# Performance work log

Hardware: AMD Instinct MI355X
Metric: run time of the kernel (lower is better)

The kernel has to match this reference:

```python
import jax, jax.numpy as jnp
import numpy as np

B, M, H = 8192, 512, 1024
CORRUPTION_LEN = int(0.6 * M)  # int(corruption_rate * input_dim)


def setup_inputs() -> dict:
    key = jax.random.key(0)
    ks = jax.random.split(key, 10)
    anchor = jax.random.normal(ks[0], (B, M), jnp.float32)
    random_sample = jax.random.normal(ks[1], (B, M), jnp.float32)
    # per-row random permutation -> exactly CORRUPTION_LEN corrupted features per row
    u = jax.random.uniform(ks[2], (B, M))
    ranks = jnp.argsort(jnp.argsort(u, axis=1), axis=1)  # rank of each column in a random permutation
    corruption_mask = ranks < CORRUPTION_LEN
    s_in = 1.0 / np.sqrt(M)
    s_h = 1.0 / np.sqrt(H)
    enc_w0 = jax.random.normal(ks[3], (M, H), jnp.float32) * s_in
    enc_b0 = jnp.full((H,), 0.01, jnp.float32)
    enc_w = jax.random.normal(ks[4], (3, H, H), jnp.float32) * s_h
    enc_b = jnp.full((3, H), 0.01, jnp.float32)
    head_w = jax.random.normal(ks[5], (2, H, H), jnp.float32) * s_h
    head_b = jnp.full((2, H), 0.01, jnp.float32)
    return {
        "anchor": anchor,
        "random_sample": random_sample,
        "corruption_mask": corruption_mask,
        "enc_w0": enc_w0,
        "enc_b0": enc_b0,
        "enc_w": enc_w,
        "enc_b": enc_b,
        "head_w": head_w,
        "head_b": head_b,
    }


def _mlp(x, w0, b0, ws, bs):
    # first dense + relu
    h = jax.nn.relu(x @ w0 + b0)
    # remaining dense + relu layers (small fixed count)
    for i in range(ws.shape[0]):
        h = jax.nn.relu(h @ ws[i] + bs[i])
    return h


def _embed(x, enc_w0, enc_b0, enc_w, enc_b, head_w, head_b):
    h = _mlp(x, enc_w0, enc_b0, enc_w, enc_b)          # encoder: 4 dense+relu
    h = jax.nn.relu(h @ head_w[0] + head_b[0])          # head: 2 dense+relu
    h = jax.nn.relu(h @ head_w[1] + head_b[1])
    return h


def reference(anchor, random_sample, corruption_mask, enc_w0, enc_b0, enc_w, enc_b, head_w, head_b):
    positive = jnp.where(corruption_mask, random_sample, anchor)
    emb_anchor = _embed(anchor, enc_w0, enc_b0, enc_w, enc_b, head_w, head_b)
    emb_positive = _embed(positive, enc_w0, enc_b0, enc_w, enc_b, head_w, head_b)
    return (emb_anchor, emb_positive)
```

## Files before the change

### kernel.cpp

```cpp
#include <hip/hip_runtime.h>
#include <hip/hip_bf16.h>
#include <stdint.h>


typedef __bf16 bf16x8 __attribute__((ext_vector_type(8)));
typedef float  f32x4  __attribute__((ext_vector_type(4)));
typedef unsigned short u16x8 __attribute__((ext_vector_type(8)));

__device__ __forceinline__ void gload_lds16(const void* g, void* l) {
  __builtin_amdgcn_global_load_lds(
      (const __attribute__((address_space(1))) uint32_t*)g,
      (__attribute__((address_space(3))) uint32_t*)l, 16, 0, 0);
}

__device__ __forceinline__ void fsplit(float v, uint16_t& ho, uint16_t& lo) {
  __bf16 hb = (__bf16)v;
  float  r  = v - (float)hb;
  __bf16 lb = (__bf16)r;
  ho = __builtin_bit_cast(uint16_t, hb);
  lo = __builtin_bit_cast(uint16_t, lb);
}

__global__ void detect_mask_kernel(const uint8_t* __restrict__ mask,
                                   int* __restrict__ flag) {
  if (threadIdx.x == 0 && blockIdx.x == 0) {
    uint32_t or_hi = 0;
    for (int i = 0; i < 256; ++i)
      or_hi |= ((const uint32_t*)mask)[i] & 0xFFFFFF00u;
    *flag = (or_hi != 0) ? 1 : 0;
  }
}

__global__ void pack_kernel(const float* __restrict__ anchor,
                            const float* __restrict__ rnd,
                            const uint8_t* __restrict__ mask,
                            const int* __restrict__ mask_is_bytes,
                            uint16_t* __restrict__ Xop) {
  int t = blockIdx.x * 256 + threadIdx.x;
  int row = t >> 6;
  int idx = t & 63;
  int g = idx >> 2, c = idx & 3;
  int kbase = idx * 8;
  const float4* ap = (const float4*)(anchor + (size_t)row * 512 + kbase);
  const float4* rp = (const float4*)(rnd + (size_t)row * 512 + kbase);
  float a[8], r[8];
  *(float4*)&a[0] = ap[0]; *(float4*)&a[4] = ap[1];
  *(float4*)&r[0] = rp[0]; *(float4*)&r[4] = rp[1];
  uint32_t mb;
  if (*mask_is_bytes) {
    const uint32_t* mp = (const uint32_t*)(mask + (size_t)row * 512 + kbase);
    uint32_t w0 = mp[0], w1 = mp[1];
    mb = 0;
#pragma unroll
    for (int j = 0; j < 4; ++j) {
      mb |= ((w0 >> (8 * j)) & 1u) << j;
      mb |= ((w1 >> (8 * j)) & 1u) << (4 + j);
    }
  } else {
    const int* mi = (const int*)mask + (size_t)row * 512 + kbase;
    int4 m0 = ((const int4*)mi)[0], m1 = ((const int4*)mi)[1];
    mb = (m0.x ? 1u : 0) | (m0.y ? 2u : 0) | (m0.z ? 4u : 0) | (m0.w ? 8u : 0) |
         (m1.x ? 16u : 0) | (m1.y ? 32u : 0) | (m1.z ? 64u : 0) | (m1.w ? 128u : 0);
  }
  u16x8 ah, al, ph, pl;
#pragma unroll
  for (int j = 0; j < 8; ++j) {
    uint16_t h, lo;
    fsplit(a[j], h, lo); ah[j] = h; al[j] = lo;
    float pv = ((mb >> j) & 1u) ? r[j] : a[j];
    fsplit(pv, h, lo); ph[j] = h; pl[j] = lo;
  }
  int s = row & 7;
  size_t base = ((size_t)row * 16 + g) * 64;
  *(u16x8*)(Xop + base + (size_t)((c ^ s)) * 8) = ah;
  *(u16x8*)(Xop + base + (size_t)(((c + 4) ^ s)) * 8) = al;
  size_t pbase = ((size_t)(row + 8192) * 16 + g) * 64;
  *(u16x8*)(Xop + pbase + (size_t)((c ^ s)) * 8) = ph;
  *(u16x8*)(Xop + pbase + (size_t)(((c + 4) ^ s)) * 8) = pl;
}

__global__ void wprep_kernel(const float* __restrict__ W,
                             uint16_t* __restrict__ Bop, int K) {
  __shared__ float tbuf[32][33];
  int g = blockIdx.x, n0 = blockIdx.y * 32;
  int tid = threadIdx.x;
#pragma unroll
  for (int i = 0; i < 4; ++i)
    tbuf[(tid >> 5) + i * 8][tid & 31] =
        W[((size_t)g * 32 + (tid >> 5) + i * 8) * 1024 + n0 + (tid & 31)];
  __syncthreads();
  if (tid < 128) {
    int nl = tid >> 2, c = tid & 3;
    int n = n0 + nl, s = n & 7;
    u16x8 hi, lo;
#pragma unroll
    for (int j = 0; j < 8; ++j) {
      uint16_t h, l2;
      fsplit(tbuf[c * 8 + j][nl], h, l2);
      hi[j] = h; lo[j] = l2;
    }
    size_t base = ((size_t)n * (K / 32) + g) * 64;
    *(u16x8*)(Bop + base + (size_t)((c ^ s)) * 8) = hi;
    *(u16x8*)(Bop + base + (size_t)(((c + 4) ^ s)) * 8) = lo;
  }
}

__device__ __forceinline__ void mfma_row(f32x4* accrow, bf16x8 aH, bf16x8 aL,
                                         const bf16x8* bh, const bf16x8* bl) {
#pragma unroll
  for (int n = 0; n < 4; ++n) {
    accrow[n] = __builtin_amdgcn_mfma_f32_16x16x32_bf16(aH, bh[n], accrow[n], 0, 0, 0);
    accrow[n] = __builtin_amdgcn_mfma_f32_16x16x32_bf16(aH, bl[n], accrow[n], 0, 0, 0);
    accrow[n] = __builtin_amdgcn_mfma_f32_16x16x32_bf16(aL, bh[n], accrow[n], 0, 0, 0);
  }
}

template <int K, bool LAST>
__global__ __launch_bounds__(512, 2) void gemm_kernel(
    const uint16_t* __restrict__ Aop, const uint16_t* __restrict__ Bop,
    const float* __restrict__ bias,
    uint16_t* __restrict__ Yop, float* __restrict__ Yf) {
  constexpr int KG = K / 32;
  __shared__ uint16_t sA[2][256 * 64];
  __shared__ uint16_t sB[2][256 * 64];

  int bid = blockIdx.x;
  int xcd = bid & 7, lid = bid >> 3;
  int tm = xcd * 8 + (lid >> 2), tn = lid & 3;
  const int brow = tm * 256, bcol = tn * 256;

  const int tid = threadIdx.x;
  const int l = tid & 63, w = tid >> 6;
  const int wr = w >> 2, wc = w & 3;
  const int l15 = l & 15, c16 = l >> 4;

  f32x4 acc[8][4];
#pragma unroll
  for (int m = 0; m < 8; ++m)
#pragma unroll
    for (int n = 0; n < 4; ++n) acc[m][n] = 0;

#define STAGE_A(g_, buf_)                                                     \
  _Pragma("unroll") for (int i = 0; i < 4; ++i) {                             \
    int row_ = i * 64 + (tid >> 3);                                           \
    gload_lds16(Aop + ((size_t)(brow + row_) * KG + (g_)) * 64 + (tid & 7) * 8,\
                &sA[buf_][i * 4096 + tid * 8]);                               \
  }
#define STAGE_B(g_, buf_)                                                     \
  _Pragma("unroll") for (int i = 0; i < 4; ++i) {                             \
    int row_ = i * 64 + (tid >> 3);                                           \
    gload_lds16(Bop + ((size_t)(bcol + row_) * KG + (g_)) * 64 + (tid & 7) * 8,\
                &sB[buf_][i * 4096 + tid * 8]);                               \
  }
#define READ_A(mm, aH, aL)                                                    \
  {                                                                           \
    int fr_ = wr * 128 + (mm)*16 + l15;                                       \
    const uint16_t* rp_ = pA + fr_ * 64;                                      \
    aH = *(const bf16x8*)(rp_ + ((c16 ^ (fr_ & 7))) * 8);                     \
    aL = *(const bf16x8*)(rp_ + (((c16 + 4) ^ (fr_ & 7))) * 8);               \
  }
#define BARRIER() __builtin_amdgcn_s_barrier()
#define VM0()                                                                 \
  asm volatile("s_waitcnt vmcnt(0)" ::: "memory");                            \
  __builtin_amdgcn_sched_barrier(0)

  STAGE_A(0, 0)
  STAGE_B(0, 0)
  VM0();
  BARRIER();

  int cur = 0;
#pragma unroll 1
  for (int g = 0; g < KG; ++g) {
    const uint16_t* pA = &sA[cur][0];
    const uint16_t* pB = &sB[cur][0];
    const bool pf = (g + 1 < KG);
    const int nxt = cur ^ 1;

    if (pf) { STAGE_A(g + 1, nxt) }

    bf16x8 bh[4], bl[4];
#pragma unroll
    for (int n = 0; n < 4; ++n) {
      int fc = wc * 64 + n * 16 + l15;
      const uint16_t* rp = pB + fc * 64;
      bh[n] = *(const bf16x8*)(rp + ((c16 ^ (fc & 7))) * 8);
      bl[n] = *(const bf16x8*)(rp + (((c16 + 4) ^ (fc & 7))) * 8);
    }
    bf16x8 a0h, a0l, a1h, a1l, a2h, a2l, a3h, a3l;
    READ_A(0, a0h, a0l)
    READ_A(1, a1h, a1l)
    READ_A(2, a2h, a2l)
    READ_A(3, a3h, a3l)
    __builtin_amdgcn_s_setprio(1);
    mfma_row(acc[0], a0h, a0l, bh, bl);
    mfma_row(acc[1], a1h, a1l, bh, bl);
    __builtin_amdgcn_s_setprio(0);
    if (pf) { STAGE_B(g + 1, nxt) }
    READ_A(4, a0h, a0l)
    READ_A(5, a1h, a1l)
    __builtin_amdgcn_s_setprio(1);
    mfma_row(acc[2], a2h, a2l, bh, bl);
    mfma_row(acc[3], a3h, a3l, bh, bl);
    __builtin_amdgcn_s_setprio(0);
    READ_A(6, a2h, a2l)
    READ_A(7, a3h, a3l)
    __builtin_amdgcn_s_setprio(1);
    mfma_row(acc[4], a0h, a0l, bh, bl);
    mfma_row(acc[5], a1h, a1l, bh, bl);
    mfma_row(acc[6], a2h, a2l, bh, bl);
    mfma_row(acc[7], a3h, a3l, bh, bl);
    __builtin_amdgcn_s_setprio(0);

    VM0();
    BARRIER();
    cur = nxt;
  }

  float bb[4];
  int colg[4], colc[4], cole[4];
#pragma unroll
  for (int n = 0; n < 4; ++n) {
    int col = bcol + wc * 64 + n * 16 + l15;
    bb[n] = bias[col];
    colg[n] = col >> 5; colc[n] = (col >> 3) & 3; cole[n] = col & 7;
  }
#pragma unroll
  for (int m = 0; m < 8; ++m) {
#pragma unroll
    for (int j = 0; j < 4; ++j) {
      int rowY = brow + wr * 128 + m * 16 + c16 * 4 + j;
      int s = rowY & 7;
#pragma unroll
      for (int n = 0; n < 4; ++n) {
        float v = acc[m][n][j] + bb[n];
        v = v > 0.f ? v : 0.f;
        if (LAST) {
          Yf[(size_t)rowY * 1024 + bcol + wc * 64 + n * 16 + l15] = v;
        } else {
          uint16_t h, lo2;
          fsplit(v, h, lo2);
          size_t base = ((size_t)rowY * 32 + colg[n]) * 64;
          Yop[base + (size_t)((colc[n] ^ s)) * 8 + cole[n]] = h;
          Yop[base + (size_t)(((colc[n] + 4) ^ s)) * 8 + cole[n]] = lo2;
        }
      }
    }
  }
#undef STAGE_A
#undef STAGE_B
#undef READ_A
#undef BARRIER
#undef VM0
}

extern "C" void kernel_launch(void* const* d_in, const int* in_sizes, int n_in,
                              void* d_out, int out_size, void* d_ws, size_t ws_size,
                              hipStream_t stream) {
  (void)in_sizes; (void)n_in; (void)out_size; (void)ws_size;
  const float*   anchor = (const float*)d_in[0];
  const float*   rnd    = (const float*)d_in[1];
  const uint8_t* mask   = (const uint8_t*)d_in[2];
  const float*   enc_w0 = (const float*)d_in[3];
  const float*   enc_b0 = (const float*)d_in[4];
  const float*   enc_w  = (const float*)d_in[5];
  const float*   enc_b  = (const float*)d_in[6];
  const float*   head_w = (const float*)d_in[7];
  const float*   head_b = (const float*)d_in[8];
  float* out = (float*)d_out;

  const size_t WSZ0 = (size_t)512 * 2048;
  const size_t WSZ1 = (size_t)1024 * 2048;
  uint16_t* Wop = (uint16_t*)d_ws;
  size_t WOFF[6];
  WOFF[0] = 0;
  WOFF[1] = WSZ0;
  for (int i = 2; i < 6; ++i) WOFF[i] = WOFF[i - 1] + WSZ1;
  uint16_t* Xop = Wop + WOFF[5] + WSZ1;
  uint16_t* Yop = Xop + (size_t)16384 * 1024;
  int* mflag = (int*)(Yop + (size_t)16384 * 2048);
  uint16_t* Zop = (uint16_t*)d_out;

  detect_mask_kernel<<<1, 64, 0, stream>>>(mask, mflag);

  pack_kernel<<<2048, 256, 0, stream>>>(anchor, rnd, mask, mflag, Xop);

  wprep_kernel<<<dim3(16, 32), 256, 0, stream>>>(enc_w0, Wop + WOFF[0], 512);
  for (int i = 0; i < 3; ++i)
    wprep_kernel<<<dim3(32, 32), 256, 0, stream>>>(enc_w + (size_t)i * 1048576,
                                                   Wop + WOFF[1 + i], 1024);
  for (int i = 0; i < 2; ++i)
    wprep_kernel<<<dim3(32, 32), 256, 0, stream>>>(head_w + (size_t)i * 1048576,
                                                   Wop + WOFF[4 + i], 1024);

  dim3 g(256), b(512);
  gemm_kernel<512,  false><<<g, b, 0, stream>>>(Xop, Wop + WOFF[0], enc_b0,        Yop, nullptr);
  gemm_kernel<1024, false><<<g, b, 0, stream>>>(Yop, Wop + WOFF[1], enc_b,         Zop, nullptr);
  gemm_kernel<1024, false><<<g, b, 0, stream>>>(Zop, Wop + WOFF[2], enc_b + 1024,  Yop, nullptr);
  gemm_kernel<1024, false><<<g, b, 0, stream>>>(Yop, Wop + WOFF[3], enc_b + 2048,  Zop, nullptr);
  gemm_kernel<1024, false><<<g, b, 0, stream>>>(Zop, Wop + WOFF[4], head_b,        Yop, nullptr);
  gemm_kernel<1024, true ><<<g, b, 0, stream>>>(Yop, Wop + WOFF[5], head_b + 1024, nullptr, out);
}
```

Before: 627.1 us.

## Switch GEMM to 128x128 tiles with 32x32x16 MFMA and ping-pong barriers

Shrinks the GEMM block tile from 256x256 with 512 threads to 128x128 with 256 threads. Each wave now computes a 64x64 sub-tile with 32x32x16 bf16 MFMAs instead of 16x16x32, and the grid grows fourfold. Extra barriers and lgkmcnt waits are added between the LDS fragment reads and the MFMA clusters, so that waves in a block alternate between memory and compute phases. Smaller tiles lower the arithmetic intensity per block and raise global and L2 traffic, in exchange for more resident blocks and fewer registers per wave.

Measured after the change: 784.1 us. +25.0%, slower.

```diff
diff --git a/kernel.cpp b/kernel.cpp
--- a/kernel.cpp
+++ b/kernel.cpp
@@ -4,7 +4,7 @@
 
 
 typedef __bf16 bf16x8 __attribute__((ext_vector_type(8)));
-typedef float  f32x4  __attribute__((ext_vector_type(4)));
+typedef float  f32x16 __attribute__((ext_vector_type(16)));
 typedef unsigned short u16x8 __attribute__((ext_vector_type(8)));
 
 __device__ __forceinline__ void gload_lds16(const void* g, void* l) {
@@ -105,64 +105,62 @@
   }
 }
 
-__device__ __forceinline__ void mfma_row(f32x4* accrow, bf16x8 aH, bf16x8 aL,
-                                         const bf16x8* bh, const bf16x8* bl) {
-#pragma unroll
-  for (int n = 0; n < 4; ++n) {
-    accrow[n] = __builtin_amdgcn_mfma_f32_16x16x32_bf16(aH, bh[n], accrow[n], 0, 0, 0);
-    accrow[n] = __builtin_amdgcn_mfma_f32_16x16x32_bf16(aH, bl[n], accrow[n], 0, 0, 0);
-    accrow[n] = __builtin_amdgcn_mfma_f32_16x16x32_bf16(aL, bh[n], accrow[n], 0, 0, 0);
-  }
-}
-
 template <int K, bool LAST>
-__global__ __launch_bounds__(512, 2) void gemm_kernel(
+__global__ __launch_bounds__(256, 2) void gemm_kernel(
     const uint16_t* __restrict__ Aop, const uint16_t* __restrict__ Bop,
     const float* __restrict__ bias,
     uint16_t* __restrict__ Yop, float* __restrict__ Yf) {
   constexpr int KG = K / 32;
-  __shared__ uint16_t sA[2][256 * 64];
-  __shared__ uint16_t sB[2][256 * 64];
+  __shared__ uint16_t sA[2][128 * 64];
+  __shared__ uint16_t sB[2][128 * 64];
 
   int bid = blockIdx.x;
   int xcd = bid & 7, lid = bid >> 3;
-  int tm = xcd * 8 + (lid >> 2), tn = lid & 3;
-  const int brow = tm * 256, bcol = tn * 256;
+  int tm = xcd * 16 + (lid >> 3), tn = lid & 7;
+  const int brow = tm * 128, bcol = tn * 128;
 
   const int tid = threadIdx.x;
   const int l = tid & 63, w = tid >> 6;
-  const int wr = w >> 2, wc = w & 3;
-  const int l15 = l & 15, c16 = l >> 4;
-
-  f32x4 acc[8][4];
-#pragma unroll
-  for (int m = 0; m < 8; ++m)
-#pragma unroll
-    for (int n = 0; n < 4; ++n) acc[m][n] = 0;
+  const int wr = w >> 1, wc = w & 1;
+  const int l31 = l & 31, lh = l >> 5;
+
+  f32x16 acc[2][2];
+#pragma unroll
+  for (int m = 0; m < 2; ++m)
+#pragma unroll
+    for (int n = 0; n < 2; ++n) acc[m][n] = 0;
 
 #define STAGE_A(g_, buf_)                                                     \
   _Pragma("unroll") for (int i = 0; i < 4; ++i) {                             \
-    int row_ = i * 64 + (tid >> 3);                                           \
+    int row_ = i * 32 + (tid >> 3);                                           \
     gload_lds16(Aop + ((size_t)(brow + row_) * KG + (g_)) * 64 + (tid & 7) * 8,\
-                &sA[buf_][i * 4096 + tid * 8]);                               \
+                &sA[buf_][i * 2048 + tid * 8]);                               \
   }
 #define STAGE_B(g_, buf_)                                                     \
   _Pragma("unroll") for (int i = 0; i < 4; ++i) {                             \
-    int row_ = i * 64 + (tid >> 3);                                           \
+    int row_ = i * 32 + (tid >> 3);                                           \
     gload_lds16(Bop + ((size_t)(bcol + row_) * KG + (g_)) * 64 + (tid & 7) * 8,\
-                &sB[buf_][i * 4096 + tid * 8]);                               \
-  }
-#define READ_A(mm, aH, aL)                                                    \
+                &sB[buf_][i * 2048 + tid * 8]);                               \
+  }
+#define READ_FRAG(p_, r_, kh, fH, fL)                                         \
   {                                                                           \
-    int fr_ = wr * 128 + (mm)*16 + l15;                                       \
-    const uint16_t* rp_ = pA + fr_ * 64;                                      \
-    aH = *(const bf16x8*)(rp_ + ((c16 ^ (fr_ & 7))) * 8);                     \
-    aL = *(const bf16x8*)(rp_ + (((c16 + 4) ^ (fr_ & 7))) * 8);               \
+    int rr_ = (r_);                                                           \
+    const uint16_t* rp_ = (p_) + rr_ * 64;                                    \
+    int c_ = (kh)*2 + lh, s_ = rr_ & 7;                                       \
+    fH = *(const bf16x8*)(rp_ + ((c_ ^ s_)) * 8);                             \
+    fL = *(const bf16x8*)(rp_ + (((c_ + 4) ^ s_)) * 8);                       \
   }
 #define BARRIER() __builtin_amdgcn_s_barrier()
+#define LGKM0()                                                               \
+  asm volatile("s_waitcnt lgkmcnt(0)" ::: "memory");                          \
+  __builtin_amdgcn_sched_barrier(0)
 #define VM0()                                                                 \
   asm volatile("s_waitcnt vmcnt(0)" ::: "memory");                            \
   __builtin_amdgcn_sched_barrier(0)
+#define MFMA3(mt, nt, aH, aL, bH, bL)                                         \
+  acc[mt][nt] = __builtin_amdgcn_mfma_f32_32x32x16_bf16(aH, bH, acc[mt][nt], 0, 0, 0); \
+  acc[mt][nt] = __builtin_amdgcn_mfma_f32_32x32x16_bf16(aH, bL, acc[mt][nt], 0, 0, 0); \
+  acc[mt][nt] = __builtin_amdgcn_mfma_f32_32x32x16_bf16(aL, bH, acc[mt][nt], 0, 0, 0);
 
   STAGE_A(0, 0)
   STAGE_B(0, 0)
@@ -179,79 +177,85 @@
 
     if (pf) { STAGE_A(g + 1, nxt) }
 
-    bf16x8 bh[4], bl[4];
-#pragma unroll
-    for (int n = 0; n < 4; ++n) {
-      int fc = wc * 64 + n * 16 + l15;
-      const uint16_t* rp = pB + fc * 64;
-      bh[n] = *(const bf16x8*)(rp + ((c16 ^ (fc & 7))) * 8);
-      bl[n] = *(const bf16x8*)(rp + (((c16 + 4) ^ (fc & 7))) * 8);
-    }
-    bf16x8 a0h, a0l, a1h, a1l, a2h, a2l, a3h, a3l;
-    READ_A(0, a0h, a0l)
-    READ_A(1, a1h, a1l)
-    READ_A(2, a2h, a2l)
-    READ_A(3, a3h, a3l)
+    bf16x8 bh[2][2], bl[2][2];
+#pragma unroll
+    for (int nt = 0; nt < 2; ++nt)
+#pragma unroll
+      for (int kh = 0; kh < 2; ++kh)
+        READ_FRAG(pB, wc * 64 + nt * 32 + l31, kh, bh[nt][kh], bl[nt][kh])
+    bf16x8 a0h[2], a0l[2];
+#pragma unroll
+    for (int kh = 0; kh < 2; ++kh)
+      READ_FRAG(pA, wr * 64 + 0 * 32 + l31, kh, a0h[kh], a0l[kh])
+    BARRIER();
+    LGKM0();
     __builtin_amdgcn_s_setprio(1);
-    mfma_row(acc[0], a0h, a0l, bh, bl);
-    mfma_row(acc[1], a1h, a1l, bh, bl);
+#pragma unroll
+    for (int kh = 0; kh < 2; ++kh) {
+      MFMA3(0, 0, a0h[kh], a0l[kh], bh[0][kh], bl[0][kh])
+      MFMA3(0, 1, a0h[kh], a0l[kh], bh[1][kh], bl[1][kh])
+    }
     __builtin_amdgcn_s_setprio(0);
     if (pf) { STAGE_B(g + 1, nxt) }
-    READ_A(4, a0h, a0l)
-    READ_A(5, a1h, a1l)
+    BARRIER();
+
+    bf16x8 a1h[2], a1l[2];
+#pragma unroll
+    for (int kh = 0; kh < 2; ++kh)
+      READ_FRAG(pA, wr * 64 + 1 * 32 + l31, kh, a1h[kh], a1l[kh])
+    BARRIER();
+    LGKM0();
     __builtin_amdgcn_s_setprio(1);
-    mfma_row(acc[2], a2h, a2l, bh, bl);
-    mfma_row(acc[3], a3h, a3l, bh, bl);
+#pragma unroll
+    for (int kh = 0; kh < 2; ++kh) {
+      MFMA3(1, 0, a1h[kh], a1l[kh], bh[0][kh], bl[0][kh])
+      MFMA3(1, 1, a1h[kh], a1l[kh], bh[1][kh], bl[1][kh])
+    }
     __builtin_amdgcn_s_setprio(0);
-    READ_A(6, a2h, a2l)
-    READ_A(7, a3h, a3l)
-    __builtin_amdgcn_s_setprio(1);
-    mfma_row(acc[4], a0h, a0l, bh, bl);
-    mfma_row(acc[5], a1h, a1l, bh, bl);
-    mfma_row(acc[6], a2h, a2l, bh, bl);
-    mfma_row(acc[7], a3h, a3l, bh, bl);
-    __builtin_amdgcn_s_setprio(0);
-
     VM0();
     BARRIER();
     cur = nxt;
   }
 
-  float bb[4];
-  int colg[4], colc[4], cole[4];
-#pragma unroll
-  for (int n = 0; n < 4; ++n) {
-    int col = bcol + wc * 64 + n * 16 + l15;
+  float bb[2];
+  int colg[2];
+  const int colc_s = (l31 >> 3) & 3;
+  const int cole = l & 7;
+#pragma unroll
+  for (int n = 0; n < 2; ++n) {
+    int col = bcol + wc * 64 + n * 32 + l31;
     bb[n] = bias[col];
-    colg[n] = col >> 5; colc[n] = (col >> 3) & 3; cole[n] = col & 7;
-  }
-#pragma unroll
-  for (int m = 0; m < 8; ++m) {
-#pragma unroll
-    for (int j = 0; j < 4; ++j) {
-      int rowY = brow + wr * 128 + m * 16 + c16 * 4 + j;
+    colg[n] = col >> 5;
+  }
+#pragma unroll
+  for (int m = 0; m < 2; ++m) {
+#pragma unroll
+    for (int reg = 0; reg < 16; ++reg) {
+      int rowY = brow + wr * 64 + m * 32 + (reg & 3) + 8 * (reg >> 2) + 4 * lh;
       int s = rowY & 7;
 #pragma unroll
-      for (int n = 0; n < 4; ++n) {
-        float v = acc[m][n][j] + bb[n];
+      for (int n = 0; n < 2; ++n) {
+        float v = acc[m][n][reg] + bb[n];
         v = v > 0.f ? v : 0.f;
         if (LAST) {
-          Yf[(size_t)rowY * 1024 + bcol + wc * 64 + n * 16 + l15] = v;
+          Yf[(size_t)rowY * 1024 + bcol + wc * 64 + n * 32 + l31] = v;
         } else {
           uint16_t h, lo2;
           fsplit(v, h, lo2);
           size_t base = ((size_t)rowY * 32 + colg[n]) * 64;
-          Yop[base + (size_t)((colc[n] ^ s)) * 8 + cole[n]] = h;
-          Yop[base + (size_t)(((colc[n] + 4) ^ s)) * 8 + cole[n]] = lo2;
+          Yop[base + (size_t)((colc_s ^ s)) * 8 + cole] = h;
+          Yop[base + (size_t)(((colc_s + 4) ^ s)) * 8 + cole] = lo2;
         }
       }
     }
   }
 #undef STAGE_A
 #undef STAGE_B
-#undef READ_A
+#undef READ_FRAG
 #undef BARRIER
+#undef LGKM0
 #undef VM0
+#undef MFMA3
 }
 
 extern "C" void kernel_launch(void* const* d_in, const int* in_sizes, int n_in,
@@ -293,7 +297,7 @@
     wprep_kernel<<<dim3(32, 32), 256, 0, stream>>>(head_w + (size_t)i * 1048576,
                                                    Wop + WOFF[4 + i], 1024);
 
-  dim3 g(256), b(512);
+  dim3 g(1024), b(256);
   gemm_kernel<512,  false><<<g, b, 0, stream>>>(Xop, Wop + WOFF[0], enc_b0,        Yop, nullptr);
   gemm_kernel<1024, false><<<g, b, 0, stream>>>(Yop, Wop + WOFF[1], enc_b,         Zop, nullptr);
   gemm_kernel<1024, false><<<g, b, 0, stream>>>(Zop, Wop + WOFF[2], enc_b + 1024,  Yop, nullptr);
```
